# Performance work log

Hardware: AMD Instinct MI355X
Metric: run time of the kernel (lower is better)

Reference implementation:

```python
import jax, jax.numpy as jnp
import numpy as np

ROPE_DIM = 16      # RotaryEmbedding(dim=16)
MAX_FREQ = 256.0   # freqs_for='pixel'
NUM_HEADS = 16


def _axis_freqs(n):
    # pixel mode: base freqs = linspace(1, max_freq/2, dim//2) * pi, pos = linspace(-1, 1, n)
    base = jnp.linspace(1.0, MAX_FREQ / 2.0, ROPE_DIM // 2) * jnp.pi  # (8,)
    pos = jnp.linspace(-1.0, 1.0, n)                                   # (n,)
    f = pos[:, None] * base[None, :]                                   # (n, 8)
    return jnp.repeat(f, 2, axis=-1)                                   # (n, 16) interleaved pairs


def axial_freqs(T, H, W):
    ft = jnp.broadcast_to(_axis_freqs(T)[:, None, None, :], (T, H, W, ROPE_DIM))
    fh = jnp.broadcast_to(_axis_freqs(H)[None, :, None, :], (T, H, W, ROPE_DIM))
    fw = jnp.broadcast_to(_axis_freqs(W)[None, None, :, :], (T, H, W, ROPE_DIM))
    return jnp.concatenate([ft, fh, fw], axis=-1)  # (T, H, W, 48)


def rotate_half(x):
    # interleaved pairs: (..., d*2) -> rotate each (x1, x2) -> (-x2, x1)
    x = x.reshape(*x.shape[:-1], -1, 2)
    x1, x2 = x[..., 0], x[..., 1]
    return jnp.stack([-x2, x1], axis=-1).reshape(*x.shape[:-2], -1)


def apply_rope(freqs, t):
    # freqs: (T, H, W, rot_dim); t: (B, nh, T, H, W, hd); rotate first rot_dim dims
    rd = freqs.shape[-1]
    tm, tr = t[..., :rd], t[..., rd:]
    tm = tm * jnp.cos(freqs) + rotate_half(tm) * jnp.sin(freqs)
    return jnp.concatenate([tm, tr], axis=-1)


def setup_inputs() -> dict:
    key = jax.random.key(0)
    k1, k2, k3, k4 = jax.random.split(key, 4)
    B, N, C = 2, 2048, 1152
    return {
        "x": jax.random.normal(k1, (B, N, C), dtype=jnp.float32),
        "Wqkv": jax.random.normal(k2, (C, 3 * C), dtype=jnp.float32) * 0.02,
        "Wproj": jax.random.normal(k3, (C, C), dtype=jnp.float32) * 0.02,
        "bproj": jax.random.normal(k4, (C,), dtype=jnp.float32) * 0.02,
        "T": 8, "H": 16, "W": 16,
    }


def reference(x, Wqkv, Wproj, bproj, T, H, W):
    B, N, C = x.shape
    nh = NUM_HEADS
    hd = C // nh
    qkv = (x @ Wqkv).reshape(B, N, 3, nh, hd).transpose(2, 0, 3, 1, 4)  # (3, B, nh, N, hd)
    q, k, v = qkv[0], qkv[1], qkv[2]
    # tokens -> video grid
    q = q.reshape(B, nh, T, H, W, hd)
    k = k.reshape(B, nh, T, H, W, hd)
    freqs = axial_freqs(T, H, W)  # (T, H, W, 48)
    q = apply_rope(freqs, q).reshape(B, nh, N, hd)
    k = apply_rope(freqs, k).reshape(B, nh, N, hd)
    # SDPA (no mask, no dropout in eval / kv_cache=None path)
    scale = 1.0 / np.sqrt(hd)
    attn = jax.nn.softmax(jnp.einsum('bhqd,bhkd->bhqk', q, k) * scale, axis=-1)
    o = jnp.einsum('bhqk,bhkd->bhqd', attn, v)  # (B, nh, N, hd)
    o = o.transpose(0, 2, 1, 3).reshape(B, N, C)
    return o @ Wproj + bproj
```

## Files before the change

kernel.cpp:

```cpp
#include <hip/hip_runtime.h>
#include <hip/hip_bf16.h>

#define B_   2
#define N_   2048
#define C_   1152
#define NH   16
#define HD   72
#define HDP  96
#define HDV  80
#define KQKV 3456
#define KROW 104
#define VROW 72
#define KVB  64

typedef __attribute__((ext_vector_type(8))) short bf16x8;
typedef __attribute__((ext_vector_type(4))) float f32x4;

__device__ __forceinline__ short f2bf(float f) {
  union { float fv; unsigned int u; } v; v.fv = f;
  unsigned int r = v.u + 0x7fffu + ((v.u >> 16) & 1u);
  return (short)(r >> 16);
}

__device__ __forceinline__ float bf2f(short s) {
  union { unsigned u; float f; } v; v.u = ((unsigned)(unsigned short)s) << 16;
  return v.f;
}

__device__ __forceinline__ unsigned pack_bf16(float a, float b) {
  union { __hip_bfloat162 h; unsigned u; } c;
  c.h = __float22bfloat162_rn(make_float2(a, b));
  return c.u;
}

__device__ __forceinline__ void gload_lds16(const short* g, short* l) {
  __builtin_amdgcn_global_load_lds(
      (const __attribute__((address_space(1))) unsigned int*)g,
      (__attribute__((address_space(3))) unsigned int*)l, 16, 0, 0);
}

__global__ void cvt_bf16(const float* __restrict__ in, short* __restrict__ out, int n4) {
  int i = blockIdx.x * 256 + threadIdx.x;
  if (i < n4) {
    float4 v = ((const float4*)in)[i];
    short4 s;
    s.x = f2bf(v.x); s.y = f2bf(v.y); s.z = f2bf(v.z); s.w = f2bf(v.w);
    ((short4*)out)[i] = s;
  }
}

__global__ void transpose_cvt(const float* __restrict__ src, short* __restrict__ dst,
                              int R, int Cc) {
  __shared__ float tile[32][33];
  const int c0 = blockIdx.x * 32, r0 = blockIdx.y * 32;
  const int tx = threadIdx.x, ty = threadIdx.y;
  for (int i = ty; i < 32; i += 8)
    tile[i][tx] = src[(long)(r0 + i) * Cc + c0 + tx];
  __syncthreads();
  for (int i = ty; i < 32; i += 8)
    dst[(long)(c0 + i) * R + r0 + tx] = f2bf(tile[tx][i]);
}

template<bool BIAS, bool OBF>
__global__ __launch_bounds__(256, 2) void gemm_bt(
    const short* __restrict__ A, const short* __restrict__ Bt,
    void* __restrict__ Cv, const float* __restrict__ bias,
    int M, int N, int K) {
  __shared__ __align__(16) short As[128 * 32];
  __shared__ __align__(16) short Bs[128 * 32];
  const int t = threadIdx.x;
  const int lane = t & 63, wid = t >> 6;
  const int fr = lane & 15, fq = lane >> 4;

  int lin = blockIdx.y * gridDim.x + blockIdx.x;
  const int q8 = (int)(gridDim.x * gridDim.y) >> 3;
  lin = (lin & 7) * q8 + (lin >> 3);
  const int bm = lin / (int)gridDim.x;
  const int bn = lin - bm * (int)gridDim.x;

  const int wr = (wid >> 1) * 64, wc = (wid & 1) * 64;

  const int srow = t >> 2;
  const int scol = (t & 3) * 8;
  const short* Ag = A + (long)(bm * 128 + srow) * K + scol;
  const short* Bg = Bt + (long)(bn * 128 + srow) * K + scol;
  short* Asl = As + t * 8;
  short* Bsl = Bs + t * 8;

  f32x4 acc[4][4] = {};

  for (int kt = 0; kt < K; kt += 32) {
    gload_lds16(Ag + kt,                 Asl);
    gload_lds16(Ag + kt + (long)64 * K,  Asl + 2048);
    gload_lds16(Bg + kt,                 Bsl);
    gload_lds16(Bg + kt + (long)64 * K,  Bsl + 2048);
    asm volatile("s_waitcnt vmcnt(0)" ::: "memory");
    __syncthreads();

    bf16x8 af[4], bf[4];
    #pragma unroll
    for (int i = 0; i < 4; ++i)
      af[i] = *(const bf16x8*)(As + (wr + i * 16 + fr) * 32 + fq * 8);
    #pragma unroll
    for (int j = 0; j < 4; ++j)
      bf[j] = *(const bf16x8*)(Bs + (wc + j * 16 + fr) * 32 + fq * 8);
    #pragma unroll
    for (int i = 0; i < 4; ++i)
      #pragma unroll
      for (int j = 0; j < 4; ++j)
        acc[i][j] = __builtin_amdgcn_mfma_f32_16x16x32_bf16(af[i], bf[j], acc[i][j], 0, 0, 0);
    __syncthreads();
  }

  #pragma unroll
  for (int i = 0; i < 4; ++i) {
    #pragma unroll
    for (int j = 0; j < 4; ++j) {
      const long row0 = (long)bm * 128 + wr + i * 16 + fq * 4;
      const int col = bn * 128 + wc + j * 16 + fr;
      const float bv = BIAS ? bias[col] : 0.f;
      #pragma unroll
      for (int r = 0; r < 4; ++r) {
        const float val = acc[i][j][r] + bv;
        if constexpr (OBF)
          ((short*)Cv)[(row0 + r) * (long)N + col] = f2bf(val);
        else
          ((float*)Cv)[(row0 + r) * (long)N + col] = val;
      }
    }
  }
}

__global__ __launch_bounds__(256) void rope_pack(
    const short* __restrict__ QKV, short* __restrict__ Qp,
    short* __restrict__ Kp, short* __restrict__ Vt) {
  const int blk = blockIdx.x;
  const int nt = blk & 15;
  const int h = (blk >> 4) & 15;
  const int b = blk >> 8;
  const int t = threadIdx.x;
  const int n0 = nt * 128;
  const float qscale = 0.17002324f;
  const float PI = 3.14159265358979323846f;

  for (int which = 0; which < 2; ++which) {
    short* dst = which ? Kp : Qp;
    const float sc = which ? 1.0f : qscale;
    for (int idx = t; idx < 128 * 48; idx += 256) {
      const int r = idx / 48;
      const int p = idx - r * 48;
      const int n = n0 + r;
      float vx = 0.f, vy = 0.f;
      if (p < 36) {
        short2 v2 = *(const short2*)(QKV + ((long)(b * N_ + n)) * KQKV + which * C_ + h * HD + 2 * p);
        vx = bf2f(v2.x); vy = bf2f(v2.y);
      }
      float o0 = vx, o1 = vy;
      if (p < 24) {
        float pos;
        if (p < 8)       pos = -1.f + (2.f / 7.f)  * (float)(n >> 8);
        else if (p < 16) pos = -1.f + (2.f / 15.f) * (float)((n >> 4) & 15);
        else             pos = -1.f + (2.f / 15.f) * (float)(n & 15);
        const float base = (1.f + (127.f / 7.f) * (float)(p & 7)) * PI;
        const float f = pos * base;
        const float cs = cosf(f), sn = sinf(f);
        o0 = vx * cs - vy * sn;
        o1 = vy * cs + vx * sn;
      }
      short2 ov; ov.x = f2bf(o0 * sc); ov.y = f2bf(o1 * sc);
      *(short2*)(dst + (((long)(b * NH + h)) * N_ + n) * HDP + 2 * p) = ov;
    }
  }

  __shared__ short vt[128][82];
  for (int idx = t; idx < 128 * 40; idx += 256) {
    const int r = idx / 40, p = idx - r * 40;
    short2 v2; v2.x = 0; v2.y = 0;
    if (p < 36)
      v2 = *(const short2*)(QKV + ((long)(b * N_ + n0 + r)) * KQKV + 2 * C_ + h * HD + 2 * p);
    *(short2*)(&vt[r][2 * p]) = v2;
  }
  __syncthreads();
  for (int idx = t; idx < HDV * 128; idx += 256) {
    const int d = idx >> 7, nn = idx & 127;
    const int c = nn & 31;
    const int nsrc = (nn & 96) | (((c >> 2) & 1) * 16 + ((c >> 3) & 3) * 4 + (c & 3));
    Vt[(((long)(b * NH + h)) * HDV + d) * N_ + n0 + nn] = vt[nsrc][d];
  }
}

__global__ __launch_bounds__(256, 3) void attn(
    const short* __restrict__ Qp, const short* __restrict__ Kp,
    const short* __restrict__ Vt, short* __restrict__ Aproj) {
  __shared__ __align__(16) short Ks[2][KVB * KROW];
  __shared__ __align__(16) short Vs[2][HDV * VROW];
  int blk = blockIdx.x;
  blk = (blk & 7) * 64 + (blk >> 3);
  const int qt = blk & 15;
  const int h = (blk >> 4) & 15;
  const int b = blk >> 8;
  const int t = threadIdx.x, lane = t & 63, wid = t >> 6;
  const int fr = lane & 15, fq = lane >> 4;

  const long bh = (long)(b * NH + h);
  const short* Qg = Qp + (bh * N_ + qt * 128) * HDP;
  const short* Kg = Kp + bh * N_ * HDP;
  const short* Vg = Vt + bh * HDV * N_;

  int koff[4];
  #pragma unroll
  for (int it = 0; it < 4; ++it) {
    const int p = it * 256 + t;
    const int row = p / 13, c = p - row * 13;
    koff[it] = row * HDP + (c < 12 ? c * 8 : 0);
  }
  int voff[3];
  #pragma unroll
  for (int it = 0; it < 3; ++it) {
    const int p = it * 256 + t;
    const int row = p / 9, c = p - row * 9;
    voff[it] = row * N_ + (c < 8 ? c * 8 : 0);
  }

  bf16x8 qf[2][3];
  #pragma unroll
  for (int i = 0; i < 2; ++i)
    #pragma unroll
    for (int kk = 0; kk < 3; ++kk)
      qf[i][kk] = *(const bf16x8*)(Qg + (wid * 32 + i * 16 + fr) * HDP + kk * 32 + fq * 8);

  f32x4 accO[2][5] = {};
  float l_[2] = {0.f, 0.f};

  auto STAGE = [&](int kt, int bufi) {
    const short* Ksrc = Kg + (long)kt * KVB * HDP;
    const short* Vsrc = Vg + kt * KVB;
    short* KD = &Ks[bufi][0];
    short* VD = &Vs[bufi][0];
    #pragma unroll
    for (int it = 0; it < 4; ++it)
      if (it < 3 || t < 64)
        gload_lds16(Ksrc + koff[it], KD + (it * 256 + t) * 8);
    #pragma unroll
    for (int it = 0; it < 3; ++it)
      if (it < 2 || t < 208)
        gload_lds16(Vsrc + voff[it], VD + (it * 256 + t) * 8);
  };

  STAGE(0, 0);
  asm volatile("s_waitcnt vmcnt(0)" ::: "memory");
  __syncthreads();

  for (int kt = 0; kt < 32; ++kt) {
    const int cur = kt & 1;
    if (kt < 31) STAGE(kt + 1, cur ^ 1);
    const short* KsC = &Ks[cur][0];
    const short* VsC = &Vs[cur][0];

    f32x4 s[2][4] = {};
    __builtin_amdgcn_s_setprio(1);
    #pragma unroll
    for (int j = 0; j < 4; ++j) {
      #pragma unroll
      for (int kk = 0; kk < 3; ++kk) {
        bf16x8 kf = *(const bf16x8*)(KsC + (j * 16 + fr) * KROW + (kk * 4 + fq) * 8);
        s[0][j] = __builtin_amdgcn_mfma_f32_16x16x32_bf16(kf, qf[0][kk], s[0][j], 0, 0, 0);
        s[1][j] = __builtin_amdgcn_mfma_f32_16x16x32_bf16(kf, qf[1][kk], s[1][j], 0, 0, 0);
      }
    }
    __builtin_amdgcn_s_setprio(0);

    #pragma unroll
    for (int i = 0; i < 2; ++i) {
      float psum = 0.f;
      #pragma unroll
      for (int j = 0; j < 4; ++j)
        #pragma unroll
        for (int r = 0; r < 4; ++r) {
          const float p = __builtin_amdgcn_exp2f(s[i][j][r]);
          s[i][j][r] = p;
          psum += p;
        }
      l_[i] += psum;
    }

    __builtin_amdgcn_s_setprio(1);
    #pragma unroll
    for (int g = 0; g < 2; ++g) {
      union { unsigned u[4]; bf16x8 v; } pf0, pf1;
      pf0.u[0] = pack_bf16(s[0][2 * g][0],     s[0][2 * g][1]);
      pf0.u[1] = pack_bf16(s[0][2 * g][2],     s[0][2 * g][3]);
      pf0.u[2] = pack_bf16(s[0][2 * g + 1][0], s[0][2 * g + 1][1]);
      pf0.u[3] = pack_bf16(s[0][2 * g + 1][2], s[0][2 * g + 1][3]);
      pf1.u[0] = pack_bf16(s[1][2 * g][0],     s[1][2 * g][1]);
      pf1.u[1] = pack_bf16(s[1][2 * g][2],     s[1][2 * g][3]);
      pf1.u[2] = pack_bf16(s[1][2 * g + 1][0], s[1][2 * g + 1][1]);
      pf1.u[3] = pack_bf16(s[1][2 * g + 1][2], s[1][2 * g + 1][3]);
      #pragma unroll
      for (int jd = 0; jd < 5; ++jd) {
        bf16x8 vf = *(const bf16x8*)(VsC + (jd * 16 + fr) * VROW + (g * 4 + fq) * 8);
        accO[0][jd] = __builtin_amdgcn_mfma_f32_16x16x32_bf16(pf0.v, vf, accO[0][jd], 0, 0, 0);
        accO[1][jd] = __builtin_amdgcn_mfma_f32_16x16x32_bf16(pf1.v, vf, accO[1][jd], 0, 0, 0);
      }
    }
    __builtin_amdgcn_s_setprio(0);
    asm volatile("s_waitcnt vmcnt(0)" ::: "memory");
    __syncthreads();
  }

  #pragma unroll
  for (int i = 0; i < 2; ++i) {
    l_[i] += __shfl_xor(l_[i], 16);
    l_[i] += __shfl_xor(l_[i], 32);
  }
  float linv[2] = {1.f / l_[0], 1.f / l_[1]};
  #pragma unroll
  for (int i = 0; i < 2; ++i) {
    float li[4];
    #pragma unroll
    for (int r = 0; r < 4; ++r) li[r] = __shfl(linv[i], fq * 4 + r);
    #pragma unroll
    for (int r = 0; r < 4; ++r) {
      const long n = qt * 128 + wid * 32 + i * 16 + fq * 4 + r;
      #pragma unroll
      for (int jd = 0; jd < 5; ++jd) {
        const int d = jd * 16 + fr;
        if (d < HD)
          Aproj[((long)b * N_ + n) * C_ + h * HD + d] = f2bf(accO[i][jd][r] * li[r]);
      }
    }
  }
}

extern "C" void kernel_launch(void* const* d_in, const int* in_sizes, int n_in,
                              void* d_out, int out_size, void* d_ws, size_t ws_size,
                              hipStream_t stream) {
  const float* x     = (const float*)d_in[0];
  const float* Wqkv  = (const float*)d_in[1];
  const float* Wproj = (const float*)d_in[2];
  const float* bproj = (const float*)d_in[3];
  float* out = (float*)d_out;

  char* ws = (char*)d_ws;
  short* QKVb = (short*)ws;        size_t off = (size_t)4096 * 3456 * 2;
  short* xb  = (short*)(ws + off);  off += (size_t)4096 * 1152 * 2;
  short* Wt  = (short*)(ws + off);  off += (size_t)3456 * 1152 * 2;
  short* Wpt = (short*)(ws + off);  off += (size_t)1152 * 1152 * 2;
  short* Qp  = (short*)(ws + off);  off += (size_t)B_ * NH * N_ * HDP * 2;
  short* Kp  = (short*)(ws + off);  off += (size_t)B_ * NH * N_ * HDP * 2;
  short* Vt  = (short*)(ws + off);  off += (size_t)B_ * NH * HDV * N_ * 2;
  short* Ap  = (short*)(ws + off);  off += (size_t)4096 * 1152 * 2;

  cvt_bf16<<<(4096 * 1152 / 4 + 255) / 256, 256, 0, stream>>>(x, xb, 4096 * 1152 / 4);
  transpose_cvt<<<dim3(3456 / 32, 1152 / 32), dim3(32, 8), 0, stream>>>(Wqkv, Wt, 1152, 3456);
  transpose_cvt<<<dim3(1152 / 32, 1152 / 32), dim3(32, 8), 0, stream>>>(Wproj, Wpt, 1152, 1152);
  gemm_bt<false, true><<<dim3(3456 / 128, 4096 / 128), 256, 0, stream>>>(
      xb, Wt, (void*)QKVb, nullptr, 4096, 3456, 1152);
  rope_pack<<<B_ * NH * (N_ / 128), 256, 0, stream>>>(QKVb, Qp, Kp, Vt);
  attn<<<B_ * NH * (N_ / 128), 256, 0, stream>>>(Qp, Kp, Vt, Ap);
  gemm_bt<true, false><<<dim3(1152 / 128, 4096 / 128), 256, 0, stream>>>(
      Ap, Wpt, (void*)out, bproj, 4096, 1152, 1152);
}
```

Measured before the change: 190.2 us.

## Double-buffer GEMM LDS tiles and enlarge attention query tile per block

The GEMM kernel now stages the next K tile into a second LDS buffer while computing on the current one, overlapping global loads with MFMA work. The attention kernel processes 256 query rows per block (64 per wave) instead of 128, so each K/V tile staged in LDS is reused across twice as many queries. This halves the attention grid and raises register use, with launch bounds lowered to one block, which may reduce occupancy and leave some CUs idle.

New measurement: 204.7 us. 7.6% more time.

```diff
diff --git a/kernel.cpp b/kernel.cpp
--- a/kernel.cpp
+++ b/kernel.cpp
@@ -66,8 +66,8 @@
     const short* __restrict__ A, const short* __restrict__ Bt,
     void* __restrict__ Cv, const float* __restrict__ bias,
     int M, int N, int K) {
-  __shared__ __align__(16) short As[128 * 32];
-  __shared__ __align__(16) short Bs[128 * 32];
+  __shared__ __align__(16) short As[2][128 * 32];
+  __shared__ __align__(16) short Bs[2][128 * 32];
   const int t = threadIdx.x;
   const int lane = t & 63, wid = t >> 6;
   const int fr = lane & 15, fq = lane >> 4;
@@ -84,31 +84,39 @@
   const int scol = (t & 3) * 8;
   const short* Ag = A + (long)(bm * 128 + srow) * K + scol;
   const short* Bg = Bt + (long)(bn * 128 + srow) * K + scol;
-  short* Asl = As + t * 8;
-  short* Bsl = Bs + t * 8;
 
   f32x4 acc[4][4] = {};
 
-  for (int kt = 0; kt < K; kt += 32) {
-    gload_lds16(Ag + kt,                 Asl);
-    gload_lds16(Ag + kt + (long)64 * K,  Asl + 2048);
-    gload_lds16(Bg + kt,                 Bsl);
-    gload_lds16(Bg + kt + (long)64 * K,  Bsl + 2048);
-    asm volatile("s_waitcnt vmcnt(0)" ::: "memory");
-    __syncthreads();
+  auto STAGE = [&](int kt, int bufi) {
+    gload_lds16(Ag + kt * 32,                &As[bufi][t * 8]);
+    gload_lds16(Ag + kt * 32 + (long)64 * K, &As[bufi][2048 + t * 8]);
+    gload_lds16(Bg + kt * 32,                &Bs[bufi][t * 8]);
+    gload_lds16(Bg + kt * 32 + (long)64 * K, &Bs[bufi][2048 + t * 8]);
+  };
+
+  const int NKT = K / 32;
+  STAGE(0, 0);
+  asm volatile("s_waitcnt vmcnt(0)" ::: "memory");
+  __syncthreads();
+
+  for (int kt = 0; kt < NKT; ++kt) {
+    const int cur = kt & 1;
+    if (kt + 1 < NKT) STAGE(kt + 1, cur ^ 1);
 
     bf16x8 af[4], bf[4];
     #pragma unroll
     for (int i = 0; i < 4; ++i)
-      af[i] = *(const bf16x8*)(As + (wr + i * 16 + fr) * 32 + fq * 8);
+      af[i] = *(const bf16x8*)(&As[cur][(wr + i * 16 + fr) * 32 + fq * 8]);
     #pragma unroll
     for (int j = 0; j < 4; ++j)
-      bf[j] = *(const bf16x8*)(Bs + (wc + j * 16 + fr) * 32 + fq * 8);
+      bf[j] = *(const bf16x8*)(&Bs[cur][(wc + j * 16 + fr) * 32 + fq * 8]);
     #pragma unroll
     for (int i = 0; i < 4; ++i)
       #pragma unroll
       for (int j = 0; j < 4; ++j)
         acc[i][j] = __builtin_amdgcn_mfma_f32_16x16x32_bf16(af[i], bf[j], acc[i][j], 0, 0, 0);
+
+    asm volatile("s_waitcnt vmcnt(0)" ::: "memory");
     __syncthreads();
   }
 
@@ -189,21 +197,21 @@
   }
 }
 
-__global__ __launch_bounds__(256, 3) void attn(
+__global__ __launch_bounds__(256, 1) void attn(
     const short* __restrict__ Qp, const short* __restrict__ Kp,
     const short* __restrict__ Vt, short* __restrict__ Aproj) {
   __shared__ __align__(16) short Ks[2][KVB * KROW];
   __shared__ __align__(16) short Vs[2][HDV * VROW];
   int blk = blockIdx.x;
-  blk = (blk & 7) * 64 + (blk >> 3);
-  const int qt = blk & 15;
-  const int h = (blk >> 4) & 15;
-  const int b = blk >> 8;
+  blk = (blk & 7) * 32 + (blk >> 3);
+  const int qt = blk & 7;
+  const int h = (blk >> 3) & 15;
+  const int b = blk >> 7;
   const int t = threadIdx.x, lane = t & 63, wid = t >> 6;
   const int fr = lane & 15, fq = lane >> 4;
 
   const long bh = (long)(b * NH + h);
-  const short* Qg = Qp + (bh * N_ + qt * 128) * HDP;
+  const short* Qg = Qp + (bh * N_ + qt * 256) * HDP;
   const short* Kg = Kp + bh * N_ * HDP;
   const short* Vg = Vt + bh * HDV * N_;
 
@@ -222,15 +230,15 @@
     voff[it] = row * N_ + (c < 8 ? c * 8 : 0);
   }
 
-  bf16x8 qf[2][3];
-  #pragma unroll
-  for (int i = 0; i < 2; ++i)
+  bf16x8 qf[4][3];
+  #pragma unroll
+  for (int i = 0; i < 4; ++i)
     #pragma unroll
     for (int kk = 0; kk < 3; ++kk)
-      qf[i][kk] = *(const bf16x8*)(Qg + (wid * 32 + i * 16 + fr) * HDP + kk * 32 + fq * 8);
-
-  f32x4 accO[2][5] = {};
-  float l_[2] = {0.f, 0.f};
+      qf[i][kk] = *(const bf16x8*)(Qg + (wid * 64 + i * 16 + fr) * HDP + kk * 32 + fq * 8);
+
+  f32x4 accO[4][5] = {};
+  float l_[4] = {0.f, 0.f, 0.f, 0.f};
 
   auto STAGE = [&](int kt, int bufi) {
     const short* Ksrc = Kg + (long)kt * KVB * HDP;
@@ -257,21 +265,22 @@
     const short* KsC = &Ks[cur][0];
     const short* VsC = &Vs[cur][0];
 
-    f32x4 s[2][4] = {};
+    f32x4 s[4][4] = {};
     __builtin_amdgcn_s_setprio(1);
     #pragma unroll
     for (int j = 0; j < 4; ++j) {
       #pragma unroll
       for (int kk = 0; kk < 3; ++kk) {
         bf16x8 kf = *(const bf16x8*)(KsC + (j * 16 + fr) * KROW + (kk * 4 + fq) * 8);
-        s[0][j] = __builtin_amdgcn_mfma_f32_16x16x32_bf16(kf, qf[0][kk], s[0][j], 0, 0, 0);
-        s[1][j] = __builtin_amdgcn_mfma_f32_16x16x32_bf16(kf, qf[1][kk], s[1][j], 0, 0, 0);
+        #pragma unroll
+        for (int i = 0; i < 4; ++i)
+          s[i][j] = __builtin_amdgcn_mfma_f32_16x16x32_bf16(kf, qf[i][kk], s[i][j], 0, 0, 0);
       }
     }
     __builtin_amdgcn_s_setprio(0);
 
     #pragma unroll
-    for (int i = 0; i < 2; ++i) {
+    for (int i = 0; i < 4; ++i) {
       float psum = 0.f;
       #pragma unroll
       for (int j = 0; j < 4; ++j)
@@ -287,20 +296,20 @@
     __builtin_amdgcn_s_setprio(1);
     #pragma unroll
     for (int g = 0; g < 2; ++g) {
-      union { unsigned u[4]; bf16x8 v; } pf0, pf1;
-      pf0.u[0] = pack_bf16(s[0][2 * g][0],     s[0][2 * g][1]);
-      pf0.u[1] = pack_bf16(s[0][2 * g][2],     s[0][2 * g][3]);
-      pf0.u[2] = pack_bf16(s[0][2 * g + 1][0], s[0][2 * g + 1][1]);
-      pf0.u[3] = pack_bf16(s[0][2 * g + 1][2], s[0][2 * g + 1][3]);
-      pf1.u[0] = pack_bf16(s[1][2 * g][0],     s[1][2 * g][1]);
-      pf1.u[1] = pack_bf16(s[1][2 * g][2],     s[1][2 * g][3]);
-      pf1.u[2] = pack_bf16(s[1][2 * g + 1][0], s[1][2 * g + 1][1]);
-      pf1.u[3] = pack_bf16(s[1][2 * g + 1][2], s[1][2 * g + 1][3]);
+      union { unsigned u[4]; bf16x8 v; } pf[4];
+      #pragma unroll
+      for (int i = 0; i < 4; ++i) {
+        pf[i].u[0] = pack_bf16(s[i][2 * g][0],     s[i][2 * g][1]);
+        pf[i].u[1] = pack_bf16(s[i][2 * g][2],     s[i][2 * g][3]);
+        pf[i].u[2] = pack_bf16(s[i][2 * g + 1][0], s[i][2 * g + 1][1]);
+        pf[i].u[3] = pack_bf16(s[i][2 * g + 1][2], s[i][2 * g + 1][3]);
+      }
       #pragma unroll
       for (int jd = 0; jd < 5; ++jd) {
         bf16x8 vf = *(const bf16x8*)(VsC + (jd * 16 + fr) * VROW + (g * 4 + fq) * 8);
-        accO[0][jd] = __builtin_amdgcn_mfma_f32_16x16x32_bf16(pf0.v, vf, accO[0][jd], 0, 0, 0);
-        accO[1][jd] = __builtin_amdgcn_mfma_f32_16x16x32_bf16(pf1.v, vf, accO[1][jd], 0, 0, 0);
+        #pragma unroll
+        for (int i = 0; i < 4; ++i)
+          accO[i][jd] = __builtin_amdgcn_mfma_f32_16x16x32_bf16(pf[i].v, vf, accO[i][jd], 0, 0, 0);
       }
     }
     __builtin_amdgcn_s_setprio(0);
@@ -309,19 +318,19 @@
   }
 
   #pragma unroll
-  for (int i = 0; i < 2; ++i) {
+  for (int i = 0; i < 4; ++i) {
     l_[i] += __shfl_xor(l_[i], 16);
     l_[i] += __shfl_xor(l_[i], 32);
   }
-  float linv[2] = {1.f / l_[0], 1.f / l_[1]};
-  #pragma unroll
-  for (int i = 0; i < 2; ++i) {
+  #pragma unroll
+  for (int i = 0; i < 4; ++i) {
+    const float linv = 1.f / l_[i];
     float li[4];
     #pragma unroll
-    for (int r = 0; r < 4; ++r) li[r] = __shfl(linv[i], fq * 4 + r);
+    for (int r = 0; r < 4; ++r) li[r] = __shfl(linv, fq * 4 + r);
     #pragma unroll
     for (int r = 0; r < 4; ++r) {
-      const long n = qt * 128 + wid * 32 + i * 16 + fq * 4 + r;
+      const long n = qt * 256 + wid * 64 + i * 16 + fq * 4 + r;
       #pragma unroll
       for (int jd = 0; jd < 5; ++jd) {
         const int d = jd * 16 + fr;
@@ -357,7 +366,7 @@
   gemm_bt<false, true><<<dim3(3456 / 128, 4096 / 128), 256, 0, stream>>>(
       xb, Wt, (void*)QKVb, nullptr, 4096, 3456, 1152);
   rope_pack<<<B_ * NH * (N_ / 128), 256, 0, stream>>>(QKVb, Qp, Kp, Vt);
-  attn<<<B_ * NH * (N_ / 128), 256, 0, stream>>>(Qp, Kp, Vt, Ap);
+  attn<<<B_ * NH * (N_ / 256), 256, 0, stream>>>(Qp, Kp, Vt, Ap);
   gemm_bt<true, false><<<dim3(1152 / 128, 4096 / 128), 256, 0, stream>>>(
       Ap, Wpt, (void*)out, bproj, 4096, 1152, 1152);
 }
```

## Add 256x256 double-buffered swizzled QKV GEMM and pipeline the 128-tile GEMM

Applied to the files above, without the earlier changes.

Replaces the QKV projection GEMM with a new 512-thread kernel using 256x256 output tiles, a K-step of 64, XOR-swizzled LDS layout and double buffering. Global-to-LDS loads for the next stage are staggered across four MFMA phases. The QKV output width is padded to 3584 so it divides the 256 tile, with zero-padded weights. The existing 128-tile GEMM used for the output projection also gets double buffering and setprio around its MFMAs. The aim is more reuse per loaded tile and overlap of memory latency with compute, at the cost of extra padded work and higher LDS and register pressure.

After: 190.8 us. Within noise of the previous version (+0.3%).

```diff
diff --git a/kernel.cpp b/kernel.cpp
--- a/kernel.cpp
+++ b/kernel.cpp
@@ -8,7 +8,7 @@
 #define HD   72
 #define HDP  96
 #define HDV  80
-#define KQKV 3456
+#define QSTR 3584
 #define KROW 104
 #define VROW 72
 #define KVB  64
@@ -50,12 +50,12 @@
 }
 
 __global__ void transpose_cvt(const float* __restrict__ src, short* __restrict__ dst,
-                              int R, int Cc) {
+                              int R, int Cc, int Np) {
   __shared__ float tile[32][33];
   const int c0 = blockIdx.x * 32, r0 = blockIdx.y * 32;
   const int tx = threadIdx.x, ty = threadIdx.y;
   for (int i = ty; i < 32; i += 8)
-    tile[i][tx] = src[(long)(r0 + i) * Cc + c0 + tx];
+    tile[i][tx] = (c0 + tx < Cc) ? src[(long)(r0 + i) * Cc + c0 + tx] : 0.f;
   __syncthreads();
   for (int i = ty; i < 32; i += 8)
     dst[(long)(c0 + i) * R + r0 + tx] = f2bf(tile[tx][i]);
@@ -66,8 +66,8 @@
     const short* __restrict__ A, const short* __restrict__ Bt,
     void* __restrict__ Cv, const float* __restrict__ bias,
     int M, int N, int K) {
-  __shared__ __align__(16) short As[128 * 32];
-  __shared__ __align__(16) short Bs[128 * 32];
+  __shared__ __align__(16) short As[2][128 * 32];
+  __shared__ __align__(16) short Bs[2][128 * 32];
   const int t = threadIdx.x;
   const int lane = t & 63, wid = t >> 6;
   const int fr = lane & 15, fq = lane >> 4;
@@ -84,32 +84,44 @@
   const int scol = (t & 3) * 8;
   const short* Ag = A + (long)(bm * 128 + srow) * K + scol;
   const short* Bg = Bt + (long)(bn * 128 + srow) * K + scol;
-  short* Asl = As + t * 8;
-  short* Bsl = Bs + t * 8;
 
   f32x4 acc[4][4] = {};
 
-  for (int kt = 0; kt < K; kt += 32) {
-    gload_lds16(Ag + kt,                 Asl);
-    gload_lds16(Ag + kt + (long)64 * K,  Asl + 2048);
-    gload_lds16(Bg + kt,                 Bsl);
-    gload_lds16(Bg + kt + (long)64 * K,  Bsl + 2048);
-    asm volatile("s_waitcnt vmcnt(0)" ::: "memory");
-    __syncthreads();
+  auto STAGE = [&](int kt, int bufi) {
+    gload_lds16(Ag + kt * 32,                &As[bufi][t * 8]);
+    gload_lds16(Ag + kt * 32 + (long)64 * K, &As[bufi][2048 + t * 8]);
+    gload_lds16(Bg + kt * 32,                &Bs[bufi][t * 8]);
+    gload_lds16(Bg + kt * 32 + (long)64 * K, &Bs[bufi][2048 + t * 8]);
+  };
+
+  const int NKT = K / 32;
+  STAGE(0, 0);
+
+  for (int kt = 0; kt < NKT; ++kt) {
+    const int cur = kt & 1;
+    if (kt + 1 < NKT) {
+      STAGE(kt + 1, cur ^ 1);
+      asm volatile("s_waitcnt vmcnt(4)" ::: "memory");
+    } else {
+      asm volatile("s_waitcnt vmcnt(0)" ::: "memory");
+    }
+    __builtin_amdgcn_s_barrier();
 
     bf16x8 af[4], bf[4];
     #pragma unroll
     for (int i = 0; i < 4; ++i)
-      af[i] = *(const bf16x8*)(As + (wr + i * 16 + fr) * 32 + fq * 8);
+      af[i] = *(const bf16x8*)(&As[cur][(wr + i * 16 + fr) * 32 + fq * 8]);
     #pragma unroll
     for (int j = 0; j < 4; ++j)
-      bf[j] = *(const bf16x8*)(Bs + (wc + j * 16 + fr) * 32 + fq * 8);
+      bf[j] = *(const bf16x8*)(&Bs[cur][(wc + j * 16 + fr) * 32 + fq * 8]);
+    __builtin_amdgcn_s_setprio(1);
     #pragma unroll
     for (int i = 0; i < 4; ++i)
       #pragma unroll
       for (int j = 0; j < 4; ++j)
         acc[i][j] = __builtin_amdgcn_mfma_f32_16x16x32_bf16(af[i], bf[j], acc[i][j], 0, 0, 0);
-    __syncthreads();
+    __builtin_amdgcn_s_setprio(0);
+    __builtin_amdgcn_s_barrier();
   }
 
   #pragma unroll
@@ -127,6 +139,145 @@
         else
           ((float*)Cv)[(row0 + r) * (long)N + col] = val;
       }
+    }
+  }
+}
+
+__global__ __launch_bounds__(512, 2) void gemm_bt256(
+    const short* __restrict__ A, const short* __restrict__ Bt,
+    short* __restrict__ Cv, int M, int N, int K) {
+  __shared__ __align__(16) short As[2][256 * 64];
+  __shared__ __align__(16) short Bs[2][256 * 64];
+  const int t = threadIdx.x;
+  const int lane = t & 63, wid = t >> 6;
+  const int fr = lane & 15, fq = lane >> 4;
+  const int wm = wid >> 2, wn = wid & 3;
+  const int rx = fr & 7;
+
+  int lin = blockIdx.y * gridDim.x + blockIdx.x;
+  const int q8 = (int)(gridDim.x * gridDim.y) >> 3;
+  lin = (lin & 7) * q8 + (lin >> 3);
+  const int bm = lin / (int)gridDim.x;
+  const int bn = lin - bm * (int)gridDim.x;
+
+  int soff[4];
+  #pragma unroll
+  for (int r = 0; r < 4; ++r) {
+    const int p = r * 512 + t;
+    const int row = p >> 3, pc = p & 7;
+    soff[r] = row * K + (pc ^ (row & 7)) * 8;
+  }
+  const short* Ag = A + (long)bm * 256 * K;
+  const short* Bg = Bt + (long)bn * 256 * K;
+
+  f32x4 acc[8][4] = {};
+
+  auto STG2 = [&](int kt, int bufi, int ph) {
+    #pragma unroll
+    for (int k2 = 0; k2 < 2; ++k2) {
+      const int r = ph * 2 + k2;
+      if (r < 4)
+        gload_lds16(Ag + soff[r] + kt * 64, &As[bufi][(r * 512 + t) * 8]);
+      else
+        gload_lds16(Bg + soff[r - 4] + kt * 64, &Bs[bufi][((r - 4) * 512 + t) * 8]);
+    }
+  };
+
+  const int NKT = K / 64;
+  #pragma unroll
+  for (int ph = 0; ph < 4; ++ph) STG2(0, 0, ph);
+
+  for (int kt = 0; kt < NKT; ++kt) {
+    const int cur = kt & 1;
+    const bool pre = (kt + 1 < NKT);
+    const short* Ac = &As[cur][0];
+    const short* Bc = &Bs[cur][0];
+    bf16x8 af[4][2], bf0[2][2], bf1[2][2];
+
+    if (pre) {
+      STG2(kt + 1, cur ^ 1, 0);
+      asm volatile("s_waitcnt vmcnt(2)" ::: "memory");
+    } else {
+      asm volatile("s_waitcnt vmcnt(0)" ::: "memory");
+    }
+    __builtin_amdgcn_s_barrier();
+    #pragma unroll
+    for (int i = 0; i < 4; ++i)
+      #pragma unroll
+      for (int kk = 0; kk < 2; ++kk)
+        af[i][kk] = *(const bf16x8*)(Ac + (wm * 128 + i * 16 + fr) * 64 + (((kk * 4 + fq) ^ rx) * 8));
+    #pragma unroll
+    for (int j = 0; j < 2; ++j)
+      #pragma unroll
+      for (int kk = 0; kk < 2; ++kk)
+        bf0[j][kk] = *(const bf16x8*)(Bc + (wn * 64 + j * 16 + fr) * 64 + (((kk * 4 + fq) ^ rx) * 8));
+    __builtin_amdgcn_s_setprio(1);
+    #pragma unroll
+    for (int i = 0; i < 4; ++i)
+      #pragma unroll
+      for (int j = 0; j < 2; ++j)
+        #pragma unroll
+        for (int kk = 0; kk < 2; ++kk)
+          acc[i][j] = __builtin_amdgcn_mfma_f32_16x16x32_bf16(af[i][kk], bf0[j][kk], acc[i][j], 0, 0, 0);
+    __builtin_amdgcn_s_setprio(0);
+    __builtin_amdgcn_s_barrier();
+
+    if (pre) STG2(kt + 1, cur ^ 1, 1);
+    #pragma unroll
+    for (int j = 0; j < 2; ++j)
+      #pragma unroll
+      for (int kk = 0; kk < 2; ++kk)
+        bf1[j][kk] = *(const bf16x8*)(Bc + (wn * 64 + 32 + j * 16 + fr) * 64 + (((kk * 4 + fq) ^ rx) * 8));
+    __builtin_amdgcn_s_setprio(1);
+    #pragma unroll
+    for (int i = 0; i < 4; ++i)
+      #pragma unroll
+      for (int j = 0; j < 2; ++j)
+        #pragma unroll
+        for (int kk = 0; kk < 2; ++kk)
+          acc[i][2 + j] = __builtin_amdgcn_mfma_f32_16x16x32_bf16(af[i][kk], bf1[j][kk], acc[i][2 + j], 0, 0, 0);
+    __builtin_amdgcn_s_setprio(0);
+    __builtin_amdgcn_s_barrier();
+
+    if (pre) STG2(kt + 1, cur ^ 1, 2);
+    #pragma unroll
+    for (int i = 0; i < 4; ++i)
+      #pragma unroll
+      for (int kk = 0; kk < 2; ++kk)
+        af[i][kk] = *(const bf16x8*)(Ac + (wm * 128 + 64 + i * 16 + fr) * 64 + (((kk * 4 + fq) ^ rx) * 8));
+    __builtin_amdgcn_s_setprio(1);
+    #pragma unroll
+    for (int i = 0; i < 4; ++i)
+      #pragma unroll
+      for (int j = 0; j < 2; ++j)
+        #pragma unroll
+        for (int kk = 0; kk < 2; ++kk)
+          acc[4 + i][j] = __builtin_amdgcn_mfma_f32_16x16x32_bf16(af[i][kk], bf0[j][kk], acc[4 + i][j], 0, 0, 0);
+    __builtin_amdgcn_s_setprio(0);
+    __builtin_amdgcn_s_barrier();
+
+    if (pre) STG2(kt + 1, cur ^ 1, 3);
+    __builtin_amdgcn_s_setprio(1);
+    #pragma unroll
+    for (int i = 0; i < 4; ++i)
+      #pragma unroll
+      for (int j = 0; j < 2; ++j)
+        #pragma unroll
+        for (int kk = 0; kk < 2; ++kk)
+          acc[4 + i][2 + j] = __builtin_amdgcn_mfma_f32_16x16x32_bf16(af[i][kk], bf1[j][kk], acc[4 + i][2 + j], 0, 0, 0);
+    __builtin_amdgcn_s_setprio(0);
+    __builtin_amdgcn_s_barrier();
+  }
+
+  #pragma unroll
+  for (int mi = 0; mi < 8; ++mi) {
+    #pragma unroll
+    for (int j = 0; j < 4; ++j) {
+      const long row0 = (long)bm * 256 + wm * 128 + (mi >> 2) * 64 + (mi & 3) * 16 + fq * 4;
+      const int col = bn * 256 + wn * 64 + j * 16 + fr;
+      #pragma unroll
+      for (int r = 0; r < 4; ++r)
+        Cv[(row0 + r) * (long)N + col] = f2bf(acc[mi][j][r]);
     }
   }
 }
@@ -152,7 +303,7 @@
       const int n = n0 + r;
       float vx = 0.f, vy = 0.f;
       if (p < 36) {
-        short2 v2 = *(const short2*)(QKV + ((long)(b * N_ + n)) * KQKV + which * C_ + h * HD + 2 * p);
+        short2 v2 = *(const short2*)(QKV + ((long)(b * N_ + n)) * QSTR + which * C_ + h * HD + 2 * p);
         vx = bf2f(v2.x); vy = bf2f(v2.y);
       }
       float o0 = vx, o1 = vy;
@@ -177,7 +328,7 @@
     const int r = idx / 40, p = idx - r * 40;
     short2 v2; v2.x = 0; v2.y = 0;
     if (p < 36)
-      v2 = *(const short2*)(QKV + ((long)(b * N_ + n0 + r)) * KQKV + 2 * C_ + h * HD + 2 * p);
+      v2 = *(const short2*)(QKV + ((long)(b * N_ + n0 + r)) * QSTR + 2 * C_ + h * HD + 2 * p);
     *(short2*)(&vt[r][2 * p]) = v2;
   }
   __syncthreads();
@@ -342,9 +493,9 @@
   float* out = (float*)d_out;
 
   char* ws = (char*)d_ws;
-  short* QKVb = (short*)ws;        size_t off = (size_t)4096 * 3456 * 2;
+  short* QKVb = (short*)ws;         size_t off = (size_t)4096 * QSTR * 2;
   short* xb  = (short*)(ws + off);  off += (size_t)4096 * 1152 * 2;
-  short* Wt  = (short*)(ws + off);  off += (size_t)3456 * 1152 * 2;
+  short* Wt  = (short*)(ws + off);  off += (size_t)QSTR * 1152 * 2;
   short* Wpt = (short*)(ws + off);  off += (size_t)1152 * 1152 * 2;
   short* Qp  = (short*)(ws + off);  off += (size_t)B_ * NH * N_ * HDP * 2;
   short* Kp  = (short*)(ws + off);  off += (size_t)B_ * NH * N_ * HDP * 2;
@@ -352,10 +503,10 @@
   short* Ap  = (short*)(ws + off);  off += (size_t)4096 * 1152 * 2;
 
   cvt_bf16<<<(4096 * 1152 / 4 + 255) / 256, 256, 0, stream>>>(x, xb, 4096 * 1152 / 4);
-  transpose_cvt<<<dim3(3456 / 32, 1152 / 32), dim3(32, 8), 0, stream>>>(Wqkv, Wt, 1152, 3456);
-  transpose_cvt<<<dim3(1152 / 32, 1152 / 32), dim3(32, 8), 0, stream>>>(Wproj, Wpt, 1152, 1152);
-  gemm_bt<false, true><<<dim3(3456 / 128, 4096 / 128), 256, 0, stream>>>(
-      xb, Wt, (void*)QKVb, nullptr, 4096, 3456, 1152);
+  transpose_cvt<<<dim3(QSTR / 32, 1152 / 32), dim3(32, 8), 0, stream>>>(Wqkv, Wt, 1152, 3456, QSTR);
+  transpose_cvt<<<dim3(1152 / 32, 1152 / 32), dim3(32, 8), 0, stream>>>(Wproj, Wpt, 1152, 1152, 1152);
+  gemm_bt256<<<dim3(QSTR / 256, 4096 / 256), 512, 0, stream>>>(
+      xb, Wt, QKVb, 4096, QSTR, 1152);
   rope_pack<<<B_ * NH * (N_ / 128), 256, 0, stream>>>(QKVb, Qp, Kp, Vt);
   attn<<<B_ * NH * (N_ / 128), 256, 0, stream>>>(Qp, Kp, Vt, Ap);
   gemm_bt<true, false><<<dim3(1152 / 128, 4096 / 128), 256, 0, stream>>>(
```
